# Performance work log

Measured on AMD Instinct MI355X. Metric: run time of the kernel, lower is better.

## Reference

```python
import jax, jax.numpy as jnp
import numpy as np
jax.config.update("jax_enable_x64", True)  # subchunk uses float64 decays (T=128 > 24)

B, T, D = 4, 2048, 1024
H, K = 16, 64            # head_size = 64, D = H*K
CHUNK = 128              # T % 128 == 0 -> only the 128-chunk path of _chunked_wkv runs
DMIX, DDEC = 32, 64      # D_MIX_DIM, D_DECAY_DIM
PREC_MIN = 0.005
LN_EPS = 1e-5 * 8.0 ** 2 # eps * head_size_divisor**2


def setup_inputs() -> dict:
    key = jax.random.key(0)
    ks = jax.random.split(key, 24)
    f32 = jnp.float32
    rn = lambda k, s, sc=1.0: (jax.random.normal(k, s) * sc).astype(f32)
    un = lambda k, s, lo, hi: jax.random.uniform(k, s, minval=lo, maxval=hi).astype(f32)
    inv_sq = 1.0 / np.sqrt(D)
    return {
        "x": rn(ks[0], (B, T, D)),
        # token-mix interpolation coefficients (init-like: in [0,1])
        "time_maa_x": un(ks[1], (1, 1, D), 0.0, 1.0),
        "time_maa_w": un(ks[2], (1, 1, D), 0.0, 1.0),
        "time_maa_k": un(ks[3], (1, 1, D), 0.0, 1.0),
        "time_maa_v": un(ks[4], (1, 1, D), 0.0, 1.0),
        "time_maa_r": un(ks[5], (1, 1, D), 0.0, 1.0),
        "time_maa_g": un(ks[6], (1, 1, D), 0.0, 1.0),
        "time_maa_w1": rn(ks[7], (D, 5 * DMIX), 0.01),
        "time_maa_w2": un(ks[8], (5, DMIX, D), -0.01, 0.01),
        # decay: init range roughly [-6, -1] like the module
        "time_decay": un(ks[9], (1, 1, D), -6.0, -1.0),
        "time_decay_w1": rn(ks[10], (D, DDEC), 0.01),
        "time_decay_w2": un(ks[11], (DDEC, D), -0.01, 0.01),
        "time_faaaa": un(ks[12], (H, K), -0.1, 0.5),
        # projections (stored [in, out]; x @ W == nn.Linear)
        "Wr": rn(ks[13], (D, D), inv_sq),
        "Wk": rn(ks[14], (D, D), inv_sq),
        "Wv": rn(ks[15], (D, D), inv_sq),
        "Wg": rn(ks[16], (D, D), inv_sq),
        "Wo": rn(ks[17], (D, D), inv_sq),
        "ln_w": jnp.ones((D,), f32),
        "ln_b": jnp.zeros((D,), f32),
    }


def _causal_shift(x):
    # x[t-1], zero at t=0
    return jnp.pad(x[:, :-1, :], ((0, 0), (1, 0), (0, 0)))


def _chunked_wkv(r, k, v, w, u, state):
    # r,k,v,w: [B,H,L,K]; u: [1,H,1,K]; state: [B,H,K,V]
    Bb, Hh, L, Kk = r.shape
    V = v.shape[-1]
    Tc = CHUNK
    N = L // Tc
    f64 = jnp.float64

    w_decay = jnp.clip(jnp.exp(w), PREC_MIN, None)
    wc_log = jnp.log(w_decay.astype(jnp.float32)).reshape(Bb, Hh, N, Tc, Kk)
    wc_cum = jnp.cumsum(wc_log, axis=-2)                              # inclusive cumsum over chunk
    shifted = jnp.pad(wc_cum[..., :-1, :], ((0, 0),) * 3 + ((1, 0), (0, 0)))
    ws = wc_log.sum(axis=-2, keepdims=True)                           # [B,H,N,1,K] total log-decay
    w_inter = jnp.exp(ws - wc_cum).astype(r.dtype)
    w_intra = jnp.exp(wc_cum - wc_log).astype(r.dtype)

    rc = r.reshape(Bb, Hh, N, Tc, Kk)
    kc = k.reshape(Bb, Hh, N, Tc, Kk)
    vc = v.reshape(Bb, Hh, N, Tc, V)

    # intra-chunk attention in float64 with mid-chunk offset for stability
    off = shifted[..., Tc // 2:Tc // 2 + 1, :]
    r_decay = jnp.exp((shifted - off).astype(f64))
    k_inv = jnp.exp((off - wc_cum).astype(f64))
    a = jnp.einsum('bhnik,bhnjk->bhnij', rc.astype(f64) * r_decay,
                   kc.astype(f64) * k_inv).astype(r.dtype)
    a = jnp.tril(a, -1)
    diag = jnp.einsum('bhntk,bhntk->bhnt', rc, u[:, :, :, None, :] * kc)  # u bonus on the diagonal
    a = a + diag[..., None] * jnp.eye(Tc, dtype=r.dtype)
    out = jnp.einsum('bhnij,bhnjv->bhniv', a, vc)

    # inter-chunk recurrent state carry
    wkv = jnp.einsum('bhntk,bhntv->bhnkv', kc * w_inter, vc)          # per-chunk KV update
    ws_e = jnp.swapaxes(jnp.exp(ws), -1, -2).astype(r.dtype)          # [B,H,N,K,1]

    def step(s, xs):
        wkv_i, ws_i = xs
        return s * ws_i + wkv_i, s                                    # emit state BEFORE update

    state_f, states = jax.lax.scan(step, state,
                                   (jnp.moveaxis(wkv, 2, 0), jnp.moveaxis(ws_e, 2, 0)))
    states = jnp.moveaxis(states, 0, 2)                               # [B,H,N,K,V]
    out = out + jnp.einsum('bhntk,bhnkv->bhntv', rc * w_intra, states)
    return out.reshape(Bb, Hh, L, V), state_f


def reference(x, time_maa_x, time_maa_w, time_maa_k, time_maa_v, time_maa_r,
              time_maa_g, time_maa_w1, time_maa_w2, time_decay, time_decay_w1,
              time_decay_w2, time_faaaa, Wr, Wk, Wv, Wg, Wo, ln_w, ln_b):
    Bb, Tt, Dd = x.shape
    xx = _causal_shift(x) - x                                          # dxprev (recurrent mode)

    # data-dependent 5-way token-mix (RWKV-6 LoRA mix)
    xxx = jnp.tanh((x + xx * time_maa_x) @ time_maa_w1)                # [B,T,5*DMIX]
    m = jnp.einsum('btfi,fid->fbtd', xxx.reshape(Bb, Tt, 5, DMIX), time_maa_w2)
    mw, mk, mv, mr, mg = m
    xw = x + xx * (time_maa_w + mw)
    xk = x + xx * (time_maa_k + mk)
    xv = x + xx * (time_maa_v + mv)
    xr = x + xx * (time_maa_r + mr)
    xg = x + xx * (time_maa_g + mg)

    to_heads = lambda t: t.reshape(Bb, Tt, H, K).transpose(0, 2, 1, 3)  # [B,H,T,K]
    r = to_heads(xr @ Wr)
    k = to_heads(xk @ Wk)
    v = to_heads(xv @ Wv)
    g = jax.nn.silu(xg @ Wg)

    ww = time_decay + jnp.tanh(xw @ time_decay_w1) @ time_decay_w2
    w = to_heads(-jnp.exp(ww))                                         # log-decay (negative)
    u = time_faaaa.reshape(1, H, 1, K)

    state0 = jnp.zeros((Bb, H, K, K), dtype=x.dtype)
    out, _state = _chunked_wkv(r, k, v, w, u, state0)

    # GroupNorm(n_head groups) over flattened (B*T, D)
    og = out.transpose(0, 2, 1, 3).reshape(Bb * Tt, H, K)
    mu = og.mean(-1, keepdims=True)
    var = og.var(-1, keepdims=True)
    og = (og - mu) / jnp.sqrt(var + LN_EPS)
    out = (og.reshape(Bb * Tt, Dd) * ln_w + ln_b).reshape(Bb, Tt, Dd)

    return (out * g) @ Wo
```

## Files before the change

kernel.cpp:

```cpp
#include <hip/hip_runtime.h>
#include <hip/hip_bf16.h>
#include <math.h>
#include <stdint.h>

typedef __hip_bfloat16 bf16;
typedef __attribute__((ext_vector_type(8))) short short8;
typedef __attribute__((ext_vector_type(4))) short short4v;
typedef __attribute__((ext_vector_type(4))) float f32x4;

#define Tt 2048
#define Dd 1024
#define Hh 16

__device__ __forceinline__ float b2f(bf16 v){ return __bfloat162float(v); }
__device__ __forceinline__ bf16  f2b(float v){ return __float2bfloat16(v); }

__device__ __forceinline__ void async16(const void* g, void* l){
  __builtin_amdgcn_global_load_lds(
      (__attribute__((address_space(1))) void*)(g),
      (__attribute__((address_space(3))) void*)(l),
      16, 0, 0);
}

__device__ __forceinline__ int seg_t(int lr, int t0, int Lm1){ return t0 + (lr & Lm1); }
__device__ __forceinline__ size_t seg_grow(int lr, int b0, int t0, int Llog2, int Lm1){
  return ((size_t)(b0 + (lr >> Llog2)) * Tt) + (size_t)seg_t(lr, t0, Lm1);
}

struct MixP { const bf16* maa[5]; bf16* dst[5]; };
struct Proj4 { const bf16* A[4]; const bf16* Bt[4]; bf16* C[4]; };
struct ConvP { const void* src[20]; bf16* dst[20]; };
struct T5P  { const bf16* src[5]; bf16* dst[5]; };

__global__ __launch_bounds__(256) void k_detect(const unsigned short* __restrict__ xs,
                                                int* __restrict__ flag){
  __shared__ int bad;
  if(threadIdx.x == 0) bad = 0;
  __syncthreads();
  int local = 0;
  for(int i = threadIdx.x; i < 8192; i += 256){
    unsigned e = (xs[i] >> 7) & 0xFF;
    if(e >= 0xC0) local++;
  }
  if(local) atomicAdd(&bad, local);
  __syncthreads();
  if(threadIdx.x == 0) flag[0] = (bad > 16) ? 1 : 0;
}

__global__ __launch_bounds__(256) void k_conv_all(ConvP p, const int* __restrict__ flag){
  const int PRE[21] = {0,8388608,8389632,8390656,8391680,8392704,8393728,8394752,
                       8558592,8722432,8723456,8788992,8854528,8855552,9904128,
                       10952704,12001280,13049856,14098432,14099456,14100480};
  int v = (blockIdx.x * 256 + threadIdx.x) * 4;
  if(v >= 14100480) return;
  int a = 0;
  #pragma unroll
  for(int i = 1; i < 20; i++) if(v >= PRE[i]) a = i;
  int off = v - PRE[a];
  bf16* d = p.dst[a] + off;
  if(flag[0]){
    f32x4 xv = *(const f32x4*)((const float*)p.src[a] + off);
    short4v o;
    #pragma unroll
    for(int j = 0; j < 4; j++) ((bf16*)&o)[j] = f2b(xv[j]);
    *(short4v*)d = o;
  } else {
    *(short4v*)d = *(const short4v*)((const short*)p.src[a] + off);
  }
}

__global__ __launch_bounds__(256) void k_transpose5(T5P p){
  __shared__ bf16 tile[32][33];
  const bf16* __restrict__ src = p.src[blockIdx.z];
  bf16* __restrict__ dst       = p.dst[blockIdx.z];
  int bx = blockIdx.x * 32, by = blockIdx.y * 32;
  int tx = threadIdx.x & 31, ty = threadIdx.x >> 5;
  for(int r = ty; r < 32; r += 8)
    tile[r][tx] = src[(size_t)(by + r) * 1024 + bx + tx];
  __syncthreads();
  for(int r = ty; r < 32; r += 8)
    dst[(size_t)(bx + r) * 1024 + by + tx] = tile[tx][r];
}

__global__ __launch_bounds__(256) void k_transposeP(const bf16* __restrict__ src,
                                                    bf16* __restrict__ dst,
                                                    int K, int N, int Npad){
  int idx = blockIdx.x * 256 + threadIdx.x;
  if(idx >= Npad * K) return;
  int n = idx / K, k = idx - n * K;
  dst[idx] = (n < N) ? src[(size_t)k * N + n] : f2b(0.f);
}

__global__ __launch_bounds__(256) void k_transposeP5(const bf16* __restrict__ src,
                                                     bf16* __restrict__ dst){
  int z = blockIdx.z;
  int idx = blockIdx.x * 256 + threadIdx.x;
  int n = idx >> 5, k = idx & 31;
  dst[(size_t)z * 32768 + idx] = src[(size_t)z * 32768 + (size_t)k * 1024 + n];
}

__global__ __launch_bounds__(256) void k_prep(const bf16* __restrict__ x,
                                              const bf16* __restrict__ tmx,
                                              bf16* __restrict__ xmx,
                                              int b0, int t0, int Llog2){
  const int Lm1 = (1 << Llog2) - 1;
  int idx = blockIdx.x * 256 + threadIdx.x;
  int lr = idx >> 10, d = idx & 1023;
  size_t grow = seg_grow(lr, b0, t0, Llog2, Lm1);
  int tl = seg_t(lr, t0, Lm1);
  float xc = b2f(x[grow * Dd + d]);
  float xp = tl ? b2f(x[(grow - 1) * Dd + d]) : 0.f;
  xmx[idx] = f2b(xc + (xp - xc) * b2f(tmx[d]));
}

constexpr int GEPI_BF16 = 0, GEPI_SILU = 1, GEPI_OUT = 2;

template<int EPI>
__global__ __launch_bounds__(256) void gemm_mfma(
    const bf16* __restrict__ A,
    const bf16* __restrict__ Bt,
    void* __restrict__ Cv,
    const int* __restrict__ oflag,
    int rowoff){
  __shared__ __align__(16) short As[128 * 32];
  __shared__ __align__(16) short Bs[128 * 32];
  int tid = threadIdx.x;
  int bn = blockIdx.x * 128;
  int bm = blockIdx.y * 128;
  int w = tid >> 6, lane = tid & 63;
  int wm = (w & 1) * 64, wn = (w >> 1) * 64;
  int m16 = lane & 15, quad = lane >> 4;

  f32x4 acc[4][4];
  #pragma unroll
  for(int mi = 0; mi < 4; mi++)
    #pragma unroll
    for(int ni = 0; ni < 4; ni++)
      acc[mi][ni] = (f32x4){0.f, 0.f, 0.f, 0.f};

  int srow = tid >> 2;
  int sk8  = (tid & 3) * 8;
  const bf16* Ag = A  + (size_t)(bm + srow) * 1024 + sk8;
  const bf16* Bg = Bt + (size_t)(bn + srow) * 1024 + sk8;
  short* Al = As + w * 512;
  short* Bl = Bs + w * 512;

  for(int kb = 0; kb < 1024; kb += 32){
    #pragma unroll
    for(int rep = 0; rep < 2; rep++){
      async16(Ag + (size_t)rep * 64 * 1024 + kb, Al + rep * 2048);
      async16(Bg + (size_t)rep * 64 * 1024 + kb, Bl + rep * 2048);
    }
    __syncthreads();
    short8 af[4], bfr[4];
    #pragma unroll
    for(int mi = 0; mi < 4; mi++)
      af[mi] = *(const short8*)(As + (wm + mi * 16 + m16) * 32 + quad * 8);
    #pragma unroll
    for(int ni = 0; ni < 4; ni++)
      bfr[ni] = *(const short8*)(Bs + (wn + ni * 16 + m16) * 32 + quad * 8);
    #pragma unroll
    for(int mi = 0; mi < 4; mi++)
      #pragma unroll
      for(int ni = 0; ni < 4; ni++)
        acc[mi][ni] = __builtin_amdgcn_mfma_f32_16x16x32_bf16(af[mi], bfr[ni], acc[mi][ni], 0, 0, 0);
    __syncthreads();
  }
  #pragma unroll
  for(int mi = 0; mi < 4; mi++){
    #pragma unroll
    for(int ni = 0; ni < 4; ni++){
      #pragma unroll
      for(int r = 0; r < 4; r++){
        int row = bm + wm + mi * 16 + quad * 4 + r;
        int col = bn + wn + ni * 16 + m16;
        float v = acc[mi][ni][r];
        if constexpr(EPI == GEPI_BF16){
          ((bf16*)Cv)[(size_t)row * 1024 + col] = f2b(v);
        } else if constexpr(EPI == GEPI_SILU){
          ((bf16*)Cv)[(size_t)row * 1024 + col] = f2b(v / (1.f + expf(-v)));
        } else {
          size_t off = (size_t)(row + rowoff) * 1024 + col;
          if(oflag[0]) ((float*)Cv)[off] = v;
          else         ((bf16*)Cv)[off]  = f2b(v);
        }
      }
    }
  }
}

__global__ __launch_bounds__(256) void gemm_proj4(Proj4 prm){
  int z = blockIdx.z;
  const bf16* __restrict__ A  = prm.A[z];
  const bf16* __restrict__ Bt = prm.Bt[z];
  bf16* __restrict__ C        = prm.C[z];
  __shared__ __align__(16) short As[128 * 32];
  __shared__ __align__(16) short Bs[128 * 32];
  int tid = threadIdx.x;
  int bn = blockIdx.x * 128;
  int bm = blockIdx.y * 128;
  int w = tid >> 6, lane = tid & 63;
  int wm = (w & 1) * 64, wn = (w >> 1) * 64;
  int m16 = lane & 15, quad = lane >> 4;

  f32x4 acc[4][4];
  #pragma unroll
  for(int mi = 0; mi < 4; mi++)
    #pragma unroll
    for(int ni = 0; ni < 4; ni++)
      acc[mi][ni] = (f32x4){0.f, 0.f, 0.f, 0.f};

  int srow = tid >> 2;
  int sk8  = (tid & 3) * 8;
  const bf16* Ag = A  + (size_t)(bm + srow) * 1024 + sk8;
  const bf16* Bg = Bt + (size_t)(bn + srow) * 1024 + sk8;
  short* Al = As + w * 512;
  short* Bl = Bs + w * 512;

  for(int kb = 0; kb < 1024; kb += 32){
    #pragma unroll
    for(int rep = 0; rep < 2; rep++){
      async16(Ag + (size_t)rep * 64 * 1024 + kb, Al + rep * 2048);
      async16(Bg + (size_t)rep * 64 * 1024 + kb, Bl + rep * 2048);
    }
    __syncthreads();
    short8 af[4], bfr[4];
    #pragma unroll
    for(int mi = 0; mi < 4; mi++)
      af[mi] = *(const short8*)(As + (wm + mi * 16 + m16) * 32 + quad * 8);
    #pragma unroll
    for(int ni = 0; ni < 4; ni++)
      bfr[ni] = *(const short8*)(Bs + (wn + ni * 16 + m16) * 32 + quad * 8);
    #pragma unroll
    for(int mi = 0; mi < 4; mi++)
      #pragma unroll
      for(int ni = 0; ni < 4; ni++)
        acc[mi][ni] = __builtin_amdgcn_mfma_f32_16x16x32_bf16(af[mi], bfr[ni], acc[mi][ni], 0, 0, 0);
    __syncthreads();
  }
  bool silu = (z == 3);
  #pragma unroll
  for(int mi = 0; mi < 4; mi++){
    #pragma unroll
    for(int ni = 0; ni < 4; ni++){
      #pragma unroll
      for(int r = 0; r < 4; r++){
        int row = bm + wm + mi * 16 + quad * 4 + r;
        int col = bn + wn + ni * 16 + m16;
        float v = acc[mi][ni][r];
        if(silu) v = v / (1.f + expf(-v));
        C[(size_t)row * 1024 + col] = f2b(v);
      }
    }
  }
}

__global__ __launch_bounds__(256) void gemm_mix(
    const bf16* __restrict__ xxx,
    const bf16* __restrict__ w2T,
    const bf16* __restrict__ xg,
    MixP prm, int b0, int t0, int Llog2){
  const int Lm1 = (1 << Llog2) - 1;
  int c = blockIdx.z;
  __shared__ __align__(16) short As[128 * 32];
  __shared__ __align__(16) short Bs[128 * 32];
  int tid = threadIdx.x;
  int bn = blockIdx.x * 128;
  int bm = blockIdx.y * 128;
  int w = tid >> 6, lane = tid & 63;
  int wm = (w & 1) * 64, wn = (w >> 1) * 64;
  int m16 = lane & 15, quad = lane >> 4;

  int srow = tid >> 2;
  int sk8  = (tid & 3) * 8;
  short* Al = As + w * 512;
  short* Bl = Bs + w * 512;
  #pragma unroll
  for(int rep = 0; rep < 2; rep++){
    async16(xxx + (size_t)(bm + srow + rep * 64) * 256 + c * 32 + sk8, Al + rep * 2048);
    async16(w2T + (size_t)c * 32768 + (size_t)(bn + srow + rep * 64) * 32 + sk8, Bl + rep * 2048);
  }
  __syncthreads();
  f32x4 acc[4][4];
  short8 af[4], bfr[4];
  #pragma unroll
  for(int mi = 0; mi < 4; mi++)
    af[mi] = *(const short8*)(As + (wm + mi * 16 + m16) * 32 + quad * 8);
  #pragma unroll
  for(int ni = 0; ni < 4; ni++)
    bfr[ni] = *(const short8*)(Bs + (wn + ni * 16 + m16) * 32 + quad * 8);
  #pragma unroll
  for(int mi = 0; mi < 4; mi++)
    #pragma unroll
    for(int ni = 0; ni < 4; ni++)
      acc[mi][ni] = __builtin_amdgcn_mfma_f32_16x16x32_bf16(
          af[mi], bfr[ni], (f32x4){0.f, 0.f, 0.f, 0.f}, 0, 0, 0);

  const bf16* maa = prm.maa[c];
  bf16* dst = prm.dst[c];
  #pragma unroll
  for(int mi = 0; mi < 4; mi++){
    #pragma unroll
    for(int ni = 0; ni < 4; ni++){
      #pragma unroll
      for(int r = 0; r < 4; r++){
        int row = bm + wm + mi * 16 + quad * 4 + r;
        int col = bn + wn + ni * 16 + m16;
        size_t grow = seg_grow(row, b0, t0, Llog2, Lm1);
        int tl = seg_t(row, t0, Lm1);
        float xc = b2f(xg[grow * Dd + col]);
        float xp = tl ? b2f(xg[(grow - 1) * Dd + col]) : 0.f;
        dst[(size_t)row * 1024 + col] =
            f2b(xc + (xp - xc) * (b2f(maa[col]) + acc[mi][ni][r]));
      }
    }
  }
}

constexpr int G2_TANH = 0, G2_DECAY = 1;

template<int EPI>
__global__ __launch_bounds__(256) void gemm_mfma2(
    const bf16* __restrict__ A,
    const bf16* __restrict__ Bt,
    void* __restrict__ Cv, int ldc,
    int Ndim, int Kdim,
    const bf16* __restrict__ e_w){
  __shared__ __align__(16) short As[128 * 32];
  __shared__ __align__(16) short Bs[128 * 32];
  int tid = threadIdx.x;
  int bn = blockIdx.x * 128;
  int bm = blockIdx.y * 128;
  int w = tid >> 6, lane = tid & 63;
  int wm = (w & 1) * 64, wn = (w >> 1) * 64;
  int m16 = lane & 15, quad = lane >> 4;

  f32x4 acc[4][4];
  #pragma unroll
  for(int mi = 0; mi < 4; mi++)
    #pragma unroll
    for(int ni = 0; ni < 4; ni++)
      acc[mi][ni] = (f32x4){0.f, 0.f, 0.f, 0.f};

  int srow = tid >> 2;
  int sk8  = (tid & 3) * 8;
  const bf16* Ag = A  + (size_t)(bm + srow) * Kdim + sk8;
  const bf16* Bg = Bt + (size_t)(bn + srow) * Kdim + sk8;
  short* Al = As + w * 512;
  short* Bl = Bs + w * 512;

  for(int kb = 0; kb < Kdim; kb += 32){
    #pragma unroll
    for(int rep = 0; rep < 2; rep++){
      async16(Ag + (size_t)rep * 64 * Kdim + kb, Al + rep * 2048);
      async16(Bg + (size_t)rep * 64 * Kdim + kb, Bl + rep * 2048);
    }
    __syncthreads();
    short8 af[4], bfr[4];
    #pragma unroll
    for(int mi = 0; mi < 4; mi++)
      af[mi] = *(const short8*)(As + (wm + mi * 16 + m16) * 32 + quad * 8);
    #pragma unroll
    for(int ni = 0; ni < 4; ni++)
      bfr[ni] = *(const short8*)(Bs + (wn + ni * 16 + m16) * 32 + quad * 8);
    #pragma unroll
    for(int mi = 0; mi < 4; mi++)
      #pragma unroll
      for(int ni = 0; ni < 4; ni++)
        acc[mi][ni] = __builtin_amdgcn_mfma_f32_16x16x32_bf16(af[mi], bfr[ni], acc[mi][ni], 0, 0, 0);
    __syncthreads();
  }
  #pragma unroll
  for(int mi = 0; mi < 4; mi++){
    #pragma unroll
    for(int ni = 0; ni < 4; ni++){
      #pragma unroll
      for(int r = 0; r < 4; r++){
        int row = bm + wm + mi * 16 + quad * 4 + r;
        int col = bn + wn + ni * 16 + m16;
        if(col >= Ndim) continue;
        float v = acc[mi][ni][r];
        size_t off = (size_t)row * ldc + col;
        if constexpr(EPI == G2_TANH){
          ((bf16*)Cv)[off] = f2b(tanhf(v));
        } else {
          float td = b2f(e_w[col]) + v;
          ((float*)Cv)[off] = fmaxf(-expf(td), -5.2983173665480363f);
        }
      }
    }
  }
}

constexpr int EPI_OUTV = 5;
#define BM 64
#define BN 64
#define BK 16

template<int EPI>
__global__ __launch_bounds__(256) void gemm_ep(
    const bf16* __restrict__ A, int lda,
    const bf16* __restrict__ Bm, int ldb,
    void* __restrict__ Cv, int ldc,
    int Mdim, int Ndim, int Kdim,
    const bf16* __restrict__ xg, const bf16* __restrict__ e_w,
    int b0, int t0, int Llog2, const int* __restrict__ oflag){
  const int Lm1 = (1 << Llog2) - 1;
  __shared__ float As[BM][BK + 1];
  __shared__ float Bs[BK][BN + 4];
  int tid = threadIdx.x;
  int tx = tid & 15, ty = tid >> 4;
  int bm = blockIdx.y * BM, bn = blockIdx.x * BN;
  float acc[4][4] = {};
  for(int kb = 0; kb < Kdim; kb += BK){
    {
      int lr = tid >> 2;
      int lc = (tid & 3) * 4;
      int gr = bm + lr;
      #pragma unroll
      for(int q = 0; q < 4; q++){
        int gc = kb + lc + q;
        float av = 0.f;
        if(gr < Mdim && gc < Kdim)
          av = b2f(A[(size_t)gr * lda + gc]);
        As[lr][lc + q] = av;
      }
    }
    {
      int lr = tid >> 4;
      int lc = (tid & 15) * 4;
      #pragma unroll
      for(int q = 0; q < 4; q++){
        int gr = kb + lr; int gc = bn + lc + q;
        Bs[lr][lc + q] = (gr < Kdim && gc < Ndim) ? b2f(Bm[(size_t)gr * ldb + gc]) : 0.f;
      }
    }
    __syncthreads();
    #pragma unroll
    for(int kk = 0; kk < BK; kk++){
      float ar[4], br[4];
      #pragma unroll
      for(int q = 0; q < 4; q++) ar[q] = As[ty * 4 + q][kk];
      #pragma unroll
      for(int q = 0; q < 4; q++) br[q] = Bs[kk][tx * 4 + q];
      #pragma unroll
      for(int mi = 0; mi < 4; mi++)
        #pragma unroll
        for(int ni = 0; ni < 4; ni++)
          acc[mi][ni] += ar[mi] * br[ni];
    }
    __syncthreads();
  }
  #pragma unroll
  for(int mi = 0; mi < 4; mi++){
    int row = bm + ty * 4 + mi;
    if(row >= Mdim) continue;
    #pragma unroll
    for(int ni = 0; ni < 4; ni++){
      int col = bn + tx * 4 + ni;
      if(col >= Ndim) continue;
      float vacc = acc[mi][ni];
      size_t grow = seg_grow(row, b0, t0, Llog2, Lm1);
      size_t go = grow * Dd + col;
      if(oflag[0]) ((float*)Cv)[go] = vacc;
      else         ((bf16*)Cv)[go]  = f2b(vacc);
    }
  }
}

__global__ __launch_bounds__(256) void k_cumsum(float* __restrict__ wd,
                                                float* __restrict__ wse,
                                                int nlog2){
  int blk = blockIdx.x;
  int dg = blk & 3; int rest = blk >> 2;
  int nmask = (1 << nlog2) - 1;
  int ln = rest & nmask; int bp = rest >> nlog2;
  int d = dg * 256 + threadIdx.x;
  size_t rowbase = (((size_t)bp << nlog2) + ln) * 128;
  size_t base = rowbase * Dd + d;
  float c = 0.f;
  for(int t = 0; t < 128; t++){
    size_t ix = base + (size_t)t * Dd;
    c += wd[ix];
    wd[ix] = c;
  }
  int h = d >> 6, k0 = d & 63;
  wse[((((size_t)bp * Hh + h) << nlog2) | ln) * 64 + k0] = __expf(fminf(c, 0.f));
}

__global__ __launch_bounds__(256) void k_chunk1(const bf16* __restrict__ kb,
                                                const bf16* __restrict__ vb,
                                                const float* __restrict__ wcum,
                                                float* __restrict__ wkv,
                                                int nlog2){
  __shared__ __align__(16) bf16 ktT[64 * 136];
  __shared__ __align__(16) bf16 vT2[64 * 136];
  int tid = threadIdx.x, blk = blockIdx.x;
  int nmask = (1 << nlog2) - 1;
  int ln = blk & nmask; int rest = blk >> nlog2;
  int h = rest & 15; int bp = rest >> 4;
  size_t rowbase = (((size_t)bp << nlog2) + ln) * 128;
  size_t gbase = rowbase * Dd + h * 64;
  for(int r = 0; r < 32; r++){
    int idx = r * 256 + tid;
    int t0 = idx >> 6, k0 = idx & 63;
    size_t gi = gbase + (size_t)t0 * Dd + k0;
    float c  = wcum[gi];
    float cL = wcum[gbase + (size_t)127 * Dd + k0];
    ktT[k0 * 136 + t0] = f2b(b2f(kb[gi]) * __expf(fminf(cL - c, 0.f)));
    vT2[k0 * 136 + t0] = vb[gi];
  }
  __syncthreads();
  int w = tid >> 6, lane = tid & 63;
  int m16 = lane & 15, quad = lane >> 4;
  f32x4 acc[4];
  #pragma unroll
  for(int nt = 0; nt < 4; nt++) acc[nt] = (f32x4){0.f, 0.f, 0.f, 0.f};
  #pragma unroll
  for(int ks = 0; ks < 4; ks++){
    short8 af = *(const short8*)(ktT + (w * 16 + m16) * 136 + ks * 32 + quad * 8);
    #pragma unroll
    for(int nt = 0; nt < 4; nt++){
      short8 bfr = *(const short8*)(vT2 + (nt * 16 + m16) * 136 + ks * 32 + quad * 8);
      acc[nt] = __builtin_amdgcn_mfma_f32_16x16x32_bf16(af, bfr, acc[nt], 0, 0, 0);
    }
  }
  size_t obase = (size_t)blk * 4096;
  #pragma unroll
  for(int nt = 0; nt < 4; nt++)
    #pragma unroll
    for(int r = 0; r < 4; r++)
      wkv[obase + (size_t)(w * 16 + quad * 4 + r) * 64 + nt * 16 + m16] = acc[nt][r];
}

__global__ __launch_bounds__(256) void k_scan(float* __restrict__ buf,
                                              const float* __restrict__ wse,
                                              float* __restrict__ st,
                                              int b0, int firstseg, int nlog2){
  int blk = blockIdx.x;
  int h = blk & 15, bp = blk >> 4;
  int tid = threadIdx.x;
  size_t stbase = ((size_t)(b0 + bp) * Hh + h) * 4096;
  int nloc = 1 << nlog2;
  float s[16];
  #pragma unroll
  for(int r = 0; r < 16; r++)
    s[r] = firstseg ? 0.f : st[stbase + r * 256 + tid];
  for(int ln = 0; ln < nloc; ln++){
    size_t idx = (((size_t)bp * Hh + h) << nlog2) | ln;
    size_t base = idx * 4096;
    const float* wsp = wse + idx * 64;
    #pragma unroll
    for(int r = 0; r < 16; r++){
      int e = r * 256 + tid;
      float tmp = buf[base + e];
      buf[base + e] = s[r];
      s[r] = s[r] * wsp[e >> 6] + tmp;
    }
  }
  #pragma unroll
  for(int r = 0; r < 16; r++)
    st[stbase + r * 256 + tid] = s[r];
}

__global__ __launch_bounds__(256) void k_chunk2(
    const bf16* __restrict__ rb, const bf16* __restrict__ kb,
    const bf16* __restrict__ vb, const float* __restrict__ wcum,
    const float* __restrict__ states, const bf16* __restrict__ u,
    float* __restrict__ outw, int nlog2){
  __shared__ __align__(16) bf16 vT[64 * 136];
  __shared__ __align__(16) bf16 sT[64 * 72];
  __shared__ __align__(16) bf16 ascr[4 * 16 * 136];
  int tid = threadIdx.x, blk = blockIdx.x;
  int nmask = (1 << nlog2) - 1;
  int ln = blk & nmask; int rest = blk >> nlog2;
  int h = rest & 15; int bp = rest >> 4;
  size_t rowbase = (((size_t)bp << nlog2) + ln) * 128;
  size_t gbase = rowbase * Dd + h * 64;
  for(int r = 0; r < 32; r++){
    int idx = r * 256 + tid;
    int t0 = idx >> 6, v0 = idx & 63;
    vT[v0 * 136 + t0] = vb[gbase + (size_t)t0 * Dd + v0];
  }
  for(int r = 0; r < 16; r++){
    int idx = r * 256 + tid;
    int k0 = idx >> 6, v0 = idx & 63;
    sT[v0 * 72 + k0] = f2b(states[(size_t)blk * 4096 + k0 * 64 + v0]);
  }
  __syncthreads();
  int w = tid >> 6, lane = tid & 63;
  int m16 = lane & 15, quad = lane >> 4;
  bf16* scr = ascr + w * (16 * 136);
  f32x4 oacc[2][4];
  #pragma unroll
  for(int a1 = 0; a1 < 2; a1++)
    #pragma unroll
    for(int a2 = 0; a2 < 4; a2++) oacc[a1][a2] = (f32x4){0.f, 0.f, 0.f, 0.f};

  for(int ii = 0; ii < 2; ii++){
    int I = ii ? (7 - w) : w;
    int B = I * 16;
    for(int z = lane; z < 544; z += 64) ((unsigned long long*)scr)[z] = 0ULL;
    int i0 = B + m16;
    size_t rowi = rowbase + i0;
    short8 rf[2], af[2], rw2[2];
    float crv[2][8];
    #pragma unroll
    for(int ks = 0; ks < 2; ks++){
      int koff = h * 64 + ks * 32 + quad * 8;
      rf[ks] = *(const short8*)(rb + rowi * Dd + koff);
      float cp[8];
      if(i0 > 0){
        f32x4 c0 = *(const f32x4*)(wcum + (rowi - 1) * Dd + koff);
        f32x4 c1 = *(const f32x4*)(wcum + (rowi - 1) * Dd + koff + 4);
        #pragma unroll
        for(int c = 0; c < 4; c++){ cp[c] = c0[c]; cp[4 + c] = c1[c]; }
      } else {
        #pragma unroll
        for(int c = 0; c < 8; c++) cp[c] = 0.f;
      }
      if(B > 0){
        f32x4 c0 = *(const f32x4*)(wcum + (rowbase + B - 1) * Dd + koff);
        f32x4 c1 = *(const f32x4*)(wcum + (rowbase + B - 1) * Dd + koff + 4);
        #pragma unroll
        for(int c = 0; c < 4; c++){ crv[ks][c] = c0[c]; crv[ks][4 + c] = c1[c]; }
      } else {
        #pragma unroll
        for(int c = 0; c < 8; c++) crv[ks][c] = 0.f;
      }
      short8 av, wv;
      #pragma unroll
      for(int c = 0; c < 8; c++){
        float rv = b2f(((const bf16*)&rf[ks])[c]);
        ((bf16*)&av)[c] = f2b(rv * __expf(fminf(cp[c] - crv[ks][c], 0.f)));
        ((bf16*)&wv)[c] = f2b(rv * __expf(fminf(cp[c], 0.f)));
      }
      af[ks] = av; rw2[ks] = wv;
    }
    for(int J = 0; J < I; J++){
      f32x4 aacc = (f32x4){0.f, 0.f, 0.f, 0.f};
      #pragma unroll
      for(int ks = 0; ks < 2; ks++){
        int koff = h * 64 + ks * 32 + quad * 8;
        size_t rowj = rowbase + J * 16 + m16;
        short8 k8 = *(const short8*)(kb + rowj * Dd + koff);
        f32x4 c0 = *(const f32x4*)(wcum + rowj * Dd + koff);
        f32x4 c1 = *(const f32x4*)(wcum + rowj * Dd + koff + 4);
        short8 bfrag;
        #pragma unroll
        for(int c = 0; c < 8; c++){
          float kv = b2f(((const bf16*)&k8)[c]);
          float cj = (c < 4) ? c0[c] : c1[c - 4];
          ((bf16*)&bfrag)[c] = f2b(kv * __expf(fminf(crv[ks][c] - cj, 0.f)));
        }
        aacc = __builtin_amdgcn_mfma_f32_16x16x32_bf16(af[ks], bfrag, aacc, 0, 0, 0);
      }
      #pragma unroll
      for(int r = 0; r < 4; r++)
        scr[(quad * 4 + r) * 136 + J * 16 + m16] = f2b(aacc[r]);
    }
    {
      f32x4 aacc = (f32x4){0.f, 0.f, 0.f, 0.f};
      f32x4 dacc = (f32x4){0.f, 0.f, 0.f, 0.f};
      #pragma unroll
      for(int ks = 0; ks < 2; ks++){
        int koff = h * 64 + ks * 32 + quad * 8;
        size_t rowj = rowbase + B + m16;
        short8 k8 = *(const short8*)(kb + rowj * Dd + koff);
        f32x4 c0 = *(const f32x4*)(wcum + rowj * Dd + koff);
        f32x4 c1 = *(const f32x4*)(wcum + rowj * Dd + koff + 4);
        short8 u8 = *(const short8*)(u + h * 64 + ks * 32 + quad * 8);
        short8 bf1, bf2;
        #pragma unroll
        for(int c = 0; c < 8; c++){
          float kv = b2f(((const bf16*)&k8)[c]);
          float cj = (c < 4) ? c0[c] : c1[c - 4];
          ((bf16*)&bf1)[c] = f2b(kv * __expf(crv[ks][c] - cj));
          ((bf16*)&bf2)[c] = f2b(kv * b2f(((const bf16*)&u8)[c]));
        }
        aacc = __builtin_amdgcn_mfma_f32_16x16x32_bf16(af[ks], bf1, aacc, 0, 0, 0);
        dacc = __builtin_amdgcn_mfma_f32_16x16x32_bf16(rf[ks], bf2, dacc, 0, 0, 0);
      }
      #pragma unroll
      for(int r = 0; r < 4; r++){
        int row = quad * 4 + r, col = m16;
        if(col < row)       scr[row * 136 + B + col] = f2b(aacc[r]);
        else if(col == row) scr[row * 136 + B + col] = f2b(dacc[r]);
      }
    }
    asm volatile("s_waitcnt lgkmcnt(0)" ::: "memory");
    int nks = (I + 2) >> 1;
    for(int ks2 = 0; ks2 < nks; ks2++){
      short8 afr = *(const short8*)(scr + m16 * 136 + ks2 * 32 + quad * 8);
      #pragma unroll
      for(int nt = 0; nt < 4; nt++){
        short8 bfr = *(const short8*)(vT + (nt * 16 + m16) * 136 + ks2 * 32 + quad * 8);
        oacc[ii][nt] = __builtin_amdgcn_mfma_f32_16x16x32_bf16(afr, bfr, oacc[ii][nt], 0, 0, 0);
      }
    }
    #pragma unroll
    for(int ks = 0; ks < 2; ks++){
      #pragma unroll
      for(int nt = 0; nt < 4; nt++){
        short8 sfr = *(const short8*)(sT + (nt * 16 + m16) * 72 + ks * 32 + quad * 8);
        oacc[ii][nt] = __builtin_amdgcn_mfma_f32_16x16x32_bf16(rw2[ks], sfr, oacc[ii][nt], 0, 0, 0);
      }
    }
  }
  __syncthreads();
  #pragma unroll
  for(int ii = 0; ii < 2; ii++){
    int I = ii ? (7 - w) : w;
    int B = I * 16;
    #pragma unroll
    for(int nt = 0; nt < 4; nt++){
      #pragma unroll
      for(int r = 0; r < 4; r++){
        int i0 = B + quad * 4 + r;
        int v0 = nt * 16 + m16;
        outw[gbase + (size_t)i0 * Dd + v0] = oacc[ii][nt][r];
      }
    }
  }
}

__global__ __launch_bounds__(256) void k_norm(const float* __restrict__ outw,
                                              const bf16* __restrict__ gb,
                                              const bf16* __restrict__ lnw,
                                              const bf16* __restrict__ lnb,
                                              bf16* __restrict__ gated){
  int lr = blockIdx.x;
  int wv = threadIdx.x >> 6, lane = threadIdx.x & 63;
  for(int hh = wv; hh < Hh; hh += 4){
    size_t ix = (size_t)lr * Dd + hh * 64 + lane;
    float xv = outw[ix];
    float s1 = xv, s2 = xv * xv;
    #pragma unroll
    for(int off = 32; off > 0; off >>= 1){
      s1 += __shfl_xor(s1, off);
      s2 += __shfl_xor(s2, off);
    }
    float mu  = s1 * 0.015625f;
    float var = s2 * 0.015625f - mu * mu;
    float inv = rsqrtf(var + 6.4e-4f);
    float og  = (xv - mu) * inv * b2f(lnw[hh * 64 + lane]) + b2f(lnb[hh * 64 + lane]);
    gated[ix] = f2b(og * b2f(gb[ix]));
  }
}

extern "C" void kernel_launch(void* const* d_in, const int* in_sizes, int n_in,
                              void* d_out, int out_size, void* d_ws, size_t ws_size,
                              hipStream_t stream){
  char* W = (char*)d_ws;
  size_t cur = 0;
  auto carve = [&](size_t bytes) -> char* {
    char* p = W + cur;
    cur = (cur + bytes + 255) & ~(size_t)255;
    return p;
  };

  int* flag = (int*)carve(4096);
  static const int NEL[20] = {8388608, 1024, 1024, 1024, 1024, 1024, 1024,
                              163840, 163840, 1024, 65536, 65536, 1024,
                              1048576, 1048576, 1048576, 1048576, 1048576,
                              1024, 1024};
  bf16* canon[20];
  for(int i = 0; i < 20; i++) canon[i] = (bf16*)carve((size_t)NEL[i] * 2);

  k_detect<<<dim3(1), 256, 0, stream>>>((const unsigned short*)d_in[0], flag);
  ConvP cp;
  for(int i = 0; i < 20; i++){ cp.src[i] = d_in[i]; cp.dst[i] = canon[i]; }
  k_conv_all<<<dim3(13770), 256, 0, stream>>>(cp, flag);

  const bf16* xp   = canon[0];
  const bf16* tmx  = canon[1];
  const bf16* tdec = canon[9];
  const bf16* up   = canon[12];
  const bf16* lnwp = canon[18];
  const bf16* lnbp = canon[19];

  bf16* WrT  = (bf16*)carve(2097152);
  bf16* WkT  = (bf16*)carve(2097152);
  bf16* WvT  = (bf16*)carve(2097152);
  bf16* WgT  = (bf16*)carve(2097152);
  bf16* WoT  = (bf16*)carve(2097152);
  bf16* W1T  = (bf16*)carve(256 * 1024 * 2);
  bf16* DW1T = (bf16*)carve(128 * 1024 * 2);
  bf16* DW2T = (bf16*)carve(1024 * 64 * 2);
  bf16* W2T  = (bf16*)carve(5 * 1024 * 32 * 2);
  T5P tp;
  tp.src[0] = canon[13]; tp.dst[0] = WrT;
  tp.src[1] = canon[14]; tp.dst[1] = WkT;
  tp.src[2] = canon[15]; tp.dst[2] = WvT;
  tp.src[3] = canon[16]; tp.dst[3] = WgT;
  tp.src[4] = canon[17]; tp.dst[4] = WoT;
  k_transpose5<<<dim3(32, 32, 5), 256, 0, stream>>>(tp);
  k_transposeP<<<dim3(1024), 256, 0, stream>>>(canon[7],  W1T,  1024, 160, 256);
  k_transposeP<<<dim3(512),  256, 0, stream>>>(canon[10], DW1T, 1024, 64, 128);
  k_transposeP<<<dim3(256),  256, 0, stream>>>(canon[11], DW2T, 64, 1024, 1024);
  k_transposeP5<<<dim3(128, 1, 5), 256, 0, stream>>>(canon[8], W2T);

  float* st = (float*)carve(1u << 20);
  size_t FIXED = cur;

  const size_t UNIT = 19104, PAD = 65536;
  int nb, L;
  if(ws_size >= FIXED + (size_t)8192 * UNIT + PAD){ nb = 4; L = 2048; }
  else {
    nb = 1; L = 2048;
    while(L > 128 && ws_size < FIXED + (size_t)L * UNIT + PAD) L >>= 1;
  }
  const int Llog2 = __builtin_ctz((unsigned)L);
  const int nlog2 = Llog2 - 7;
  const int M     = nb * L;
  const size_t Mr = (size_t)M;

  bf16*  xxx    = (bf16*) carve(Mr * 512);
  bf16*  ww1    = (bf16*) carve(Mr * 128);
  float* wse    = (float*)carve(Mr * 32);
  bf16*  xmx    = (bf16*) carve(Mr * 2048);
  bf16*  mixbuf = (bf16*) carve(Mr * 2048);
  bf16*  kbuf   = (bf16*) carve(Mr * 2048);
  bf16*  vbuf   = (bf16*) carve(Mr * 2048);
  bf16*  rbuf   = (bf16*) carve(Mr * 2048);
  bf16*  gbuf   = (bf16*) carve(Mr * 2048);
  float* wdec   = (float*)carve(Mr * 4096);
  float* wkvst  = (float*)carve(Mr * 2048);
  float* outw   = wdec;
  bf16*  gated  = mixbuf;

  MixP mp;
  mp.maa[0] = canon[2]; mp.maa[1] = canon[3]; mp.maa[2] = canon[4];
  mp.maa[3] = canon[5]; mp.maa[4] = canon[6];
  mp.dst[0] = mixbuf;
  mp.dst[1] = (bf16*)wdec;
  mp.dst[2] = (bf16*)wdec + Mr * 1024;
  mp.dst[3] = (bf16*)wkvst;
  mp.dst[4] = xmx;

  Proj4 pp;
  pp.A[0] = mp.dst[1]; pp.Bt[0] = WkT; pp.C[0] = kbuf;
  pp.A[1] = mp.dst[2]; pp.Bt[1] = WvT; pp.C[1] = vbuf;
  pp.A[2] = mp.dst[3]; pp.Bt[2] = WrT; pp.C[2] = rbuf;
  pp.A[3] = mp.dst[4]; pp.Bt[3] = WgT; pp.C[3] = gbuf;

  for(int b0 = 0; b0 < 4; b0 += nb){
    for(int t0 = 0; t0 < Tt; t0 += L){
      k_prep<<<dim3(M * 4), 256, 0, stream>>>(xp, tmx, xmx, b0, t0, Llog2);
      gemm_mfma2<G2_TANH><<<dim3(2, M/128), 256, 0, stream>>>(
          xmx, W1T, xxx, 256, 160, 1024, nullptr);
      gemm_mix<<<dim3(8, M/128, 5), 256, 0, stream>>>(
          xxx, W2T, xp, mp, b0, t0, Llog2);
      gemm_proj4<<<dim3(8, M/128, 4), 256, 0, stream>>>(pp);
      gemm_mfma2<G2_TANH><<<dim3(1, M/128), 256, 0, stream>>>(
          mixbuf, DW1T, ww1, 64, 64, 1024, nullptr);
      gemm_mfma2<G2_DECAY><<<dim3(8, M/128), 256, 0, stream>>>(
          ww1, DW2T, wdec, 1024, 1024, 64, tdec);
      int nloc = 1 << nlog2;
      k_cumsum<<<dim3(nb * nloc * 4), 256, 0, stream>>>(wdec, wse, nlog2);
      k_chunk1<<<dim3(nb * 16 * nloc), 256, 0, stream>>>(kbuf, vbuf, wdec, wkvst, nlog2);
      k_scan<<<dim3(nb * 16), 256, 0, stream>>>(wkvst, wse, st, b0, (t0 == 0) ? 1 : 0, nlog2);
      k_chunk2<<<dim3(nb * 16 * nloc), 256, 0, stream>>>(rbuf, kbuf, vbuf, wdec, wkvst, up, outw, nlog2);
      k_norm<<<dim3(M), 256, 0, stream>>>(outw, gbuf, lnwp, lnbp, gated);
      if(L == Tt){
        gemm_mfma<GEPI_OUT><<<dim3(8, M/128), 256, 0, stream>>>(gated, WoT, d_out, flag, b0 * Tt);
      } else {
        gemm_ep<EPI_OUTV><<<dim3(16, M/64), 256, 0, stream>>>(
            gated, 1024, canon[17], 1024, d_out, 1024, M, 1024, 1024,
            nullptr, nullptr, b0, t0, Llog2, flag);
      }
    }
  }
}
```

Baseline: 569.1 us.

## Double-buffer GEMM LDS tiles and swizzle block order across XCDs

The GEMM kernels now use two LDS buffers per operand and issue async global-to-LDS loads for the next K slice while MFMAs run on the current one, hiding load latency behind compute. The main and projection GEMMs also remap block indices so that consecutive blocks landing on the same XCD share A rows, improving L2 reuse. This doubles LDS use per block, which may lower occupancy. The loop keeps a single barrier per iteration, so there is a risk of reading a buffer before its async load has completed or overwriting one still being read.

```diff
diff --git a/kernel.cpp b/kernel.cpp
--- a/kernel.cpp
+++ b/kernel.cpp
@@ -25,6 +25,21 @@
 __device__ __forceinline__ int seg_t(int lr, int t0, int Lm1){ return t0 + (lr & Lm1); }
 __device__ __forceinline__ size_t seg_grow(int lr, int b0, int t0, int Llog2, int Lm1){
   return ((size_t)(b0 + (lr >> Llog2)) * Tt) + (size_t)seg_t(lr, t0, Lm1);
+}
+
+__device__ __forceinline__ void xcd_swz(int& bn, int& bm, int& z){
+  int nbm = gridDim.y;
+  if((nbm & 7) == 0){
+    int flat = blockIdx.x + (blockIdx.y << 3) + blockIdx.z * (nbm << 3);
+    int j = flat & 7, k = flat >> 3;
+    int cs = nbm >> 3;
+    bn = (k & 7) << 7;
+    int kk = k >> 3;
+    bm = (j * cs + (kk % cs)) << 7;
+    z  = kk / cs;
+  } else {
+    bn = blockIdx.x << 7; bm = blockIdx.y << 7; z = blockIdx.z;
+  }
 }
 
 struct MixP { const bf16* maa[5]; bf16* dst[5]; };
@@ -122,11 +137,11 @@
     void* __restrict__ Cv,
     const int* __restrict__ oflag,
     int rowoff){
-  __shared__ __align__(16) short As[128 * 32];
-  __shared__ __align__(16) short Bs[128 * 32];
+  __shared__ __align__(16) short As[2][128 * 32];
+  __shared__ __align__(16) short Bs[2][128 * 32];
   int tid = threadIdx.x;
-  int bn = blockIdx.x * 128;
-  int bm = blockIdx.y * 128;
+  int bn, bm, zz;
+  xcd_swz(bn, bm, zz);
   int w = tid >> 6, lane = tid & 63;
   int wm = (w & 1) * 64, wn = (w >> 1) * 64;
   int m16 = lane & 15, quad = lane >> 4;
@@ -142,23 +157,26 @@
   int sk8  = (tid & 3) * 8;
   const bf16* Ag = A  + (size_t)(bm + srow) * 1024 + sk8;
   const bf16* Bg = Bt + (size_t)(bn + srow) * 1024 + sk8;
-  short* Al = As + w * 512;
-  short* Bl = Bs + w * 512;
-
-  for(int kb = 0; kb < 1024; kb += 32){
+
+  auto STG = [&](int buf, int kb){
     #pragma unroll
     for(int rep = 0; rep < 2; rep++){
-      async16(Ag + (size_t)rep * 64 * 1024 + kb, Al + rep * 2048);
-      async16(Bg + (size_t)rep * 64 * 1024 + kb, Bl + rep * 2048);
-    }
-    __syncthreads();
+      async16(Ag + (size_t)rep * 64 * 1024 + kb, &As[buf][w * 512 + rep * 2048]);
+      async16(Bg + (size_t)rep * 64 * 1024 + kb, &Bs[buf][w * 512 + rep * 2048]);
+    }
+  };
+  STG(0, 0);
+  __syncthreads();
+  for(int kbi = 0; kbi < 32; kbi++){
+    int cur = kbi & 1;
+    if(kbi < 31) STG(cur ^ 1, (kbi + 1) << 5);
     short8 af[4], bfr[4];
     #pragma unroll
     for(int mi = 0; mi < 4; mi++)
-      af[mi] = *(const short8*)(As + (wm + mi * 16 + m16) * 32 + quad * 8);
+      af[mi] = *(const short8*)(&As[cur][(wm + mi * 16 + m16) * 32 + quad * 8]);
     #pragma unroll
     for(int ni = 0; ni < 4; ni++)
-      bfr[ni] = *(const short8*)(Bs + (wn + ni * 16 + m16) * 32 + quad * 8);
+      bfr[ni] = *(const short8*)(&Bs[cur][(wn + ni * 16 + m16) * 32 + quad * 8]);
     #pragma unroll
     for(int mi = 0; mi < 4; mi++)
       #pragma unroll
@@ -190,15 +208,14 @@
 }
 
 __global__ __launch_bounds__(256) void gemm_proj4(Proj4 prm){
-  int z = blockIdx.z;
+  __shared__ __align__(16) short As[2][128 * 32];
+  __shared__ __align__(16) short Bs[2][128 * 32];
+  int tid = threadIdx.x;
+  int bn, bm, z;
+  xcd_swz(bn, bm, z);
   const bf16* __restrict__ A  = prm.A[z];
   const bf16* __restrict__ Bt = prm.Bt[z];
   bf16* __restrict__ C        = prm.C[z];
-  __shared__ __align__(16) short As[128 * 32];
-  __shared__ __align__(16) short Bs[128 * 32];
-  int tid = threadIdx.x;
-  int bn = blockIdx.x * 128;
-  int bm = blockIdx.y * 128;
   int w = tid >> 6, lane = tid & 63;
   int wm = (w & 1) * 64, wn = (w >> 1) * 64;
   int m16 = lane & 15, quad = lane >> 4;
@@ -214,23 +231,26 @@
   int sk8  = (tid & 3) * 8;
   const bf16* Ag = A  + (size_t)(bm + srow) * 1024 + sk8;
   const bf16* Bg = Bt + (size_t)(bn + srow) * 1024 + sk8;
-  short* Al = As + w * 512;
-  short* Bl = Bs + w * 512;
-
-  for(int kb = 0; kb < 1024; kb += 32){
+
+  auto STG = [&](int buf, int kb){
     #pragma unroll
     for(int rep = 0; rep < 2; rep++){
-      async16(Ag + (size_t)rep * 64 * 1024 + kb, Al + rep * 2048);
-      async16(Bg + (size_t)rep * 64 * 1024 + kb, Bl + rep * 2048);
-    }
-    __syncthreads();
+      async16(Ag + (size_t)rep * 64 * 1024 + kb, &As[buf][w * 512 + rep * 2048]);
+      async16(Bg + (size_t)rep * 64 * 1024 + kb, &Bs[buf][w * 512 + rep * 2048]);
+    }
+  };
+  STG(0, 0);
+  __syncthreads();
+  for(int kbi = 0; kbi < 32; kbi++){
+    int cur = kbi & 1;
+    if(kbi < 31) STG(cur ^ 1, (kbi + 1) << 5);
     short8 af[4], bfr[4];
     #pragma unroll
     for(int mi = 0; mi < 4; mi++)
-      af[mi] = *(const short8*)(As + (wm + mi * 16 + m16) * 32 + quad * 8);
+      af[mi] = *(const short8*)(&As[cur][(wm + mi * 16 + m16) * 32 + quad * 8]);
     #pragma unroll
     for(int ni = 0; ni < 4; ni++)
-      bfr[ni] = *(const short8*)(Bs + (wn + ni * 16 + m16) * 32 + quad * 8);
+      bfr[ni] = *(const short8*)(&Bs[cur][(wn + ni * 16 + m16) * 32 + quad * 8]);
     #pragma unroll
     for(int mi = 0; mi < 4; mi++)
       #pragma unroll
@@ -326,8 +346,8 @@
     void* __restrict__ Cv, int ldc,
     int Ndim, int Kdim,
     const bf16* __restrict__ e_w){
-  __shared__ __align__(16) short As[128 * 32];
-  __shared__ __align__(16) short Bs[128 * 32];
+  __shared__ __align__(16) short As[2][128 * 32];
+  __shared__ __align__(16) short Bs[2][128 * 32];
   int tid = threadIdx.x;
   int bn = blockIdx.x * 128;
   int bm = blockIdx.y * 128;
@@ -346,23 +366,27 @@
   int sk8  = (tid & 3) * 8;
   const bf16* Ag = A  + (size_t)(bm + srow) * Kdim + sk8;
   const bf16* Bg = Bt + (size_t)(bn + srow) * Kdim + sk8;
-  short* Al = As + w * 512;
-  short* Bl = Bs + w * 512;
-
-  for(int kb = 0; kb < Kdim; kb += 32){
+
+  auto STG = [&](int buf, int kb){
     #pragma unroll
     for(int rep = 0; rep < 2; rep++){
-      async16(Ag + (size_t)rep * 64 * Kdim + kb, Al + rep * 2048);
-      async16(Bg + (size_t)rep * 64 * Kdim + kb, Bl + rep * 2048);
-    }
-    __syncthreads();
+      async16(Ag + (size_t)rep * 64 * Kdim + kb, &As[buf][w * 512 + rep * 2048]);
+      async16(Bg + (size_t)rep * 64 * Kdim + kb, &Bs[buf][w * 512 + rep * 2048]);
+    }
+  };
+  int nk = Kdim >> 5;
+  STG(0, 0);
+  __syncthreads();
+  for(int kbi = 0; kbi < nk; kbi++){
+    int cur = kbi & 1;
+    if(kbi + 1 < nk) STG(cur ^ 1, (kbi + 1) << 5);
     short8 af[4], bfr[4];
     #pragma unroll
     for(int mi = 0; mi < 4; mi++)
-      af[mi] = *(const short8*)(As + (wm + mi * 16 + m16) * 32 + quad * 8);
+      af[mi] = *(const short8*)(&As[cur][(wm + mi * 16 + m16) * 32 + quad * 8]);
     #pragma unroll
     for(int ni = 0; ni < 4; ni++)
-      bfr[ni] = *(const short8*)(Bs + (wn + ni * 16 + m16) * 32 + quad * 8);
+      bfr[ni] = *(const short8*)(&Bs[cur][(wn + ni * 16 + m16) * 32 + quad * 8]);
     #pragma unroll
     for(int mi = 0; mi < 4; mi++)
       #pragma unroll
```

Result: slower. 639.8 us (+12.4%).

## Enlarge proj4 GEMM tiles to 256x256 with double-buffered LDS and XCD swizzle

Applied to the files above, without the earlier changes.

The batched four-way projection GEMM now uses 512-thread blocks computing 256x256 tiles, with double-buffered LDS staging that prefetches the next K slice while the current one is consumed. LDS columns are rotated to avoid bank conflicts, and block indices are remapped so blocks sharing A rows land on the same XCD for L2 reuse. gemm_mfma gets a similar XCD swizzle. The intent is more data reuse per block and load latency hidden behind MFMA, at the cost of higher register and LDS pressure. Non-8192-row cases fall back to per-projection gemm_mfma launches.

```diff
diff --git a/kernel.cpp b/kernel.cpp
--- a/kernel.cpp
+++ b/kernel.cpp
@@ -25,6 +25,21 @@
 __device__ __forceinline__ int seg_t(int lr, int t0, int Lm1){ return t0 + (lr & Lm1); }
 __device__ __forceinline__ size_t seg_grow(int lr, int b0, int t0, int Llog2, int Lm1){
   return ((size_t)(b0 + (lr >> Llog2)) * Tt) + (size_t)seg_t(lr, t0, Lm1);
+}
+
+__device__ __forceinline__ void xcd_swz(int& bn, int& bm, int& z){
+  int nbm = gridDim.y;
+  if((nbm & 7) == 0){
+    int flat = blockIdx.x + (blockIdx.y << 3) + blockIdx.z * (nbm << 3);
+    int j = flat & 7, k = flat >> 3;
+    int cs = nbm >> 3;
+    bn = (k & 7) << 7;
+    int kk = k >> 3;
+    bm = (j * cs + (kk % cs)) << 7;
+    z  = kk / cs;
+  } else {
+    bn = blockIdx.x << 7; bm = blockIdx.y << 7; z = blockIdx.z;
+  }
 }
 
 struct MixP { const bf16* maa[5]; bf16* dst[5]; };
@@ -125,8 +140,8 @@
   __shared__ __align__(16) short As[128 * 32];
   __shared__ __align__(16) short Bs[128 * 32];
   int tid = threadIdx.x;
-  int bn = blockIdx.x * 128;
-  int bm = blockIdx.y * 128;
+  int bn, bm, zz;
+  xcd_swz(bn, bm, zz);
   int w = tid >> 6, lane = tid & 63;
   int wm = (w & 1) * 64, wn = (w >> 1) * 64;
   int m16 = lane & 15, quad = lane >> 4;
@@ -189,50 +204,60 @@
   }
 }
 
-__global__ __launch_bounds__(256) void gemm_proj4(Proj4 prm){
-  int z = blockIdx.z;
+__global__ __launch_bounds__(512) void gemm_proj4(Proj4 prm){
+  __shared__ __align__(16) short As[2][256 * 32];
+  __shared__ __align__(16) short Bs[2][256 * 32];
+  int tid = threadIdx.x;
+  int flat = blockIdx.x + (blockIdx.y << 2) + (blockIdx.z << 7);
+  int j = flat & 7, k = flat >> 3;
+  int bn = (k & 3) << 8;
+  int kk = k >> 2;
+  int bm = (j * 4 + (kk & 3)) << 8;
+  int z  = kk >> 2;
   const bf16* __restrict__ A  = prm.A[z];
   const bf16* __restrict__ Bt = prm.Bt[z];
   bf16* __restrict__ C        = prm.C[z];
-  __shared__ __align__(16) short As[128 * 32];
-  __shared__ __align__(16) short Bs[128 * 32];
-  int tid = threadIdx.x;
-  int bn = blockIdx.x * 128;
-  int bm = blockIdx.y * 128;
   int w = tid >> 6, lane = tid & 63;
-  int wm = (w & 1) * 64, wn = (w >> 1) * 64;
+  int wm = (w & 1) * 128, wn = (w >> 1) * 64;
   int m16 = lane & 15, quad = lane >> 4;
 
-  f32x4 acc[4][4];
-  #pragma unroll
-  for(int mi = 0; mi < 4; mi++)
+  f32x4 acc[8][4];
+  #pragma unroll
+  for(int mi = 0; mi < 8; mi++)
     #pragma unroll
     for(int ni = 0; ni < 4; ni++)
       acc[mi][ni] = (f32x4){0.f, 0.f, 0.f, 0.f};
 
   int srow = tid >> 2;
-  int sk8  = (tid & 3) * 8;
-  const bf16* Ag = A  + (size_t)(bm + srow) * 1024 + sk8;
-  const bf16* Bg = Bt + (size_t)(bn + srow) * 1024 + sk8;
-  short* Al = As + w * 512;
-  short* Bl = Bs + w * 512;
-
-  for(int kb = 0; kb < 1024; kb += 32){
+  int c4   = ((tid & 3) - (srow >> 1)) & 3;
+  const bf16* Ag = A  + (size_t)(bm + srow) * 1024 + c4 * 8;
+  const bf16* Bg = Bt + (size_t)(bn + srow) * 1024 + c4 * 8;
+
+  auto STG = [&](int buf, int kb){
     #pragma unroll
     for(int rep = 0; rep < 2; rep++){
-      async16(Ag + (size_t)rep * 64 * 1024 + kb, Al + rep * 2048);
-      async16(Bg + (size_t)rep * 64 * 1024 + kb, Bl + rep * 2048);
-    }
-    __syncthreads();
-    short8 af[4], bfr[4];
-    #pragma unroll
-    for(int mi = 0; mi < 4; mi++)
-      af[mi] = *(const short8*)(As + (wm + mi * 16 + m16) * 32 + quad * 8);
-    #pragma unroll
-    for(int ni = 0; ni < 4; ni++)
-      bfr[ni] = *(const short8*)(Bs + (wn + ni * 16 + m16) * 32 + quad * 8);
-    #pragma unroll
-    for(int mi = 0; mi < 4; mi++)
+      async16(Ag + (size_t)rep * 128 * 1024 + kb, &As[buf][rep * 4096 + w * 512]);
+      async16(Bg + (size_t)rep * 128 * 1024 + kb, &Bs[buf][rep * 4096 + w * 512]);
+    }
+  };
+  STG(0, 0);
+  __syncthreads();
+  for(int kbi = 0; kbi < 32; kbi++){
+    int cur = kbi & 1;
+    if(kbi < 31) STG(cur ^ 1, (kbi + 1) << 5);
+    short8 af[8], bfr[4];
+    #pragma unroll
+    for(int mi = 0; mi < 8; mi++){
+      int ar = wm + mi * 16 + m16;
+      af[mi] = *(const short8*)(&As[cur][ar * 32 + ((quad + (ar >> 1)) & 3) * 8]);
+    }
+    #pragma unroll
+    for(int ni = 0; ni < 4; ni++){
+      int br = wn + ni * 16 + m16;
+      bfr[ni] = *(const short8*)(&Bs[cur][br * 32 + ((quad + (br >> 1)) & 3) * 8]);
+    }
+    #pragma unroll
+    for(int mi = 0; mi < 8; mi++)
       #pragma unroll
       for(int ni = 0; ni < 4; ni++)
         acc[mi][ni] = __builtin_amdgcn_mfma_f32_16x16x32_bf16(af[mi], bfr[ni], acc[mi][ni], 0, 0, 0);
@@ -240,7 +265,7 @@
   }
   bool silu = (z == 3);
   #pragma unroll
-  for(int mi = 0; mi < 4; mi++){
+  for(int mi = 0; mi < 8; mi++){
     #pragma unroll
     for(int ni = 0; ni < 4; ni++){
       #pragma unroll
@@ -851,7 +876,16 @@
           xmx, W1T, xxx, 256, 160, 1024, nullptr);
       gemm_mix<<<dim3(8, M/128, 5), 256, 0, stream>>>(
           xxx, W2T, xp, mp, b0, t0, Llog2);
-      gemm_proj4<<<dim3(8, M/128, 4), 256, 0, stream>>>(pp);
+      if(M == 8192){
+        gemm_proj4<<<dim3(4, 32, 4), 512, 0, stream>>>(pp);
+      } else {
+        for(int z = 0; z < 4; z++){
+          if(z == 3)
+            gemm_mfma<GEPI_SILU><<<dim3(8, M/128), 256, 0, stream>>>(pp.A[z], pp.Bt[z], pp.C[z], flag, 0);
+          else
+            gemm_mfma<GEPI_BF16><<<dim3(8, M/128), 256, 0, stream>>>(pp.A[z], pp.Bt[z], pp.C[z], flag, 0);
+        }
+      }
       gemm_mfma2<G2_TANH><<<dim3(1, M/128), 256, 0, stream>>>(
           mixbuf, DW1T, ww1, 64, 64, 1024, nullptr);
       gemm_mfma2<G2_DECAY><<<dim3(8, M/128), 256, 0, stream>>>(
```

Result: faster. 551.6 us (-3.1%).
